# Performance work log

Hardware: AMD Instinct MI355X
Metric: run time of the kernel (lower is better)

Reference implementation:

```python
import jax, jax.numpy as jnp
import numpy as np

DIM = 512
NUM_HEADS = 8
HEAD_DIM = DIM // NUM_HEADS
MAX_SIZE = 128


def setup_inputs() -> dict:
    key = jax.random.key(0)
    ks = jax.random.split(key, 13)
    B, C, H, W = 4, DIM, 128, 128
    inp = {
        "x": jax.random.normal(ks[0], (B, C, H, W), jnp.float32),
        "q_w": jax.random.normal(ks[1], (DIM, DIM), jnp.float32) * 0.02,
        "q_b": jax.random.normal(ks[2], (DIM,), jnp.float32) * 0.02,
        "k_w": jax.random.normal(ks[3], (DIM, DIM), jnp.float32) * 0.02,
        "k_b": jax.random.normal(ks[4], (DIM,), jnp.float32) * 0.02,
        "v_w": jax.random.normal(ks[5], (DIM, DIM), jnp.float32) * 0.02,
        "v_b": jax.random.normal(ks[6], (DIM,), jnp.float32) * 0.02,
        "o_w": jax.random.normal(ks[7], (DIM, DIM), jnp.float32) * 0.02,
        "o_b": jax.random.normal(ks[8], (DIM,), jnp.float32) * 0.02,
        "pos_q": jax.random.normal(ks[9], (1, NUM_HEADS, MAX_SIZE, HEAD_DIM), jnp.float32),
        "pos_k": jax.random.normal(ks[10], (1, NUM_HEADS, MAX_SIZE, HEAD_DIM), jnp.float32),
        "pos_v": jax.random.normal(ks[11], (1, NUM_HEADS, MAX_SIZE, HEAD_DIM), jnp.float32),
        "g_q": jnp.ones((1,), jnp.float32),
        "g_k": jnp.ones((1,), jnp.float32),
        "g_v1": jnp.ones((1,), jnp.float32),
        "g_v2": jnp.ones((1,), jnp.float32),
    }
    return inp


def _gated_axial_attn(x, q_w, q_b, k_w, k_b, v_w, v_b, o_w, o_b,
                      pos_q, pos_k, pos_v, g_q, g_k, g_v1, g_v2):
    B, C, H, W = x.shape
    nh, hd = NUM_HEADS, C // NUM_HEADS
    scale = hd ** (-0.5)
    # axis='width': attend along W for each (B,H) row
    xf = jnp.transpose(x, (0, 2, 3, 1)).reshape(B * H, W, C)  # (BH, W, C)

    def proj(w, b):
        y = xf @ w.T + b                       # (BH, W, C)
        return jnp.transpose(y.reshape(B * H, W, nh, hd), (0, 2, 1, 3))  # (BH, nh, W, hd)

    q = proj(q_w, q_b)
    k = proj(k_w, k_b)
    v = proj(v_w, v_b)

    pq = pos_q[0, :, :W, :]  # (nh, W, hd)
    pk = pos_k[0, :, :W, :]
    pv = pos_v[0, :, :W, :]

    # scores[i,j] = q_i.k_j + g_q * q_i.pq_j + g_k * pk_i.k_j, all scaled
    scores = jnp.einsum('bnid,bnjd->bnij', q, k)
    scores = scores + g_q[0] * jnp.einsum('bnid,njd->bnij', q, pq)
    scores = scores + g_k[0] * jnp.einsum('nid,bnjd->bnij', pk, k)
    attn = jax.nn.softmax(scores * scale, axis=-1)  # (BH, nh, W, W)

    vmix = g_v1[0] * v + g_v2[0] * pv[None]        # (BH, nh, W, hd)
    out = jnp.einsum('bnij,bnjd->bnid', attn, vmix)
    out = jnp.transpose(out, (0, 2, 1, 3)).reshape(B * H, W, C)
    out = out @ o_w.T + o_b
    return jnp.transpose(out.reshape(B, H, W, C), (0, 3, 1, 2))  # (B, C, H, W)


def reference(x, q_w, q_b, k_w, k_b, v_w, v_b, o_w, o_b,
              pos_q, pos_k, pos_v, g_q, g_k, g_v1, g_v2):
    return _gated_axial_attn(x, q_w, q_b, k_w, k_b, v_w, v_b, o_w, o_b,
                             pos_q, pos_k, pos_v, g_q, g_k, g_v1, g_v2)
```

## Files before the change

kernel.cpp:

```cpp
#include <hip/hip_runtime.h>

typedef __bf16 bf16;
typedef __attribute__((ext_vector_type(8))) __bf16 bf16x8;
typedef __attribute__((ext_vector_type(4))) __bf16 bf16x4;
typedef __attribute__((ext_vector_type(4))) float fvec4;

#define MFMA16(a, b, c) __builtin_amdgcn_mfma_f32_16x16x32_bf16(a, b, c, 0, 0, 0)

__device__ __forceinline__ void glds16(const bf16* g, bf16* l) {
  __builtin_amdgcn_global_load_lds(
      (const __attribute__((address_space(1))) void*)g,
      (__attribute__((address_space(3))) void*)l, 16, 0, 0);
}

__device__ inline fvec4 zero4() { fvec4 z = {0.f, 0.f, 0.f, 0.f}; return z; }

#define PREP_ELEMS 1245184

__global__ __launch_bounds__(512) void prep_kernel(
    const float* __restrict__ qw, const float* __restrict__ kw,
    const float* __restrict__ vw, const float* __restrict__ ow,
    const float* __restrict__ pq, const float* __restrict__ pk,
    const float* __restrict__ pv,
    const float* __restrict__ g_q, const float* __restrict__ g_k,
    const float* __restrict__ g_v2, bf16* __restrict__ dst)
{
  int i = (blockIdx.x * 512 + threadIdx.x) * 4;
  const float* s;
  float sc = 1.f;
  if      (i < 262144)  s = qw + i;
  else if (i < 524288)  s = kw + (i - 262144);
  else if (i < 786432)  s = vw + (i - 524288);
  else if (i < 1048576) s = ow + (i - 786432);
  else if (i < 1114112) { s = pq + (i - 1048576); sc = g_q[0]; }
  else if (i < 1179648) { s = pk + (i - 1114112); sc = g_k[0]; }
  else                  { s = pv + (i - 1179648); sc = g_v2[0]; }
  fvec4 v = *(const fvec4*)s;
  bf16x4 o = { (bf16)(v[0] * sc), (bf16)(v[1] * sc),
               (bf16)(v[2] * sc), (bf16)(v[3] * sc) };
  *(bf16x4*)(dst + i) = o;
}

__global__ __launch_bounds__(256) void xpose_kernel(
    const float* __restrict__ x, bf16* __restrict__ xt, int bh0)
{
  __shared__ float Xs[64 * 133];
  const int cb = blockIdx.x, lb = blockIdx.y;
  const int bh = bh0 + lb, b = bh >> 7, h = bh & 127;
  const int t = threadIdx.x;
  const float* xb = x + (size_t)b * 8388608 + (size_t)(cb * 64) * 16384 + h * 128;
  #pragma unroll
  for (int it = 0; it < 8; ++it) {
    int idx = it * 256 + t;
    int c = idx >> 5, w4 = (idx & 31) << 2;
    fvec4 v = *(const fvec4*)(xb + (size_t)c * 16384 + w4);
    #pragma unroll
    for (int j = 0; j < 4; ++j) Xs[c * 133 + w4 + j] = v[j];
  }
  __syncthreads();
  const int c0 = (t & 7) * 8, wsub = t >> 3;
  #pragma unroll
  for (int wb = 0; wb < 4; ++wb) {
    int w = wb * 32 + wsub;
    bf16x8 o;
    #pragma unroll
    for (int i = 0; i < 8; ++i) o[i] = (bf16)Xs[(c0 + i) * 133 + w];
    *(bf16x8*)(xt + ((size_t)lb * 128 + w) * 512 + cb * 64 + c0) = o;
  }
}

__global__ __launch_bounds__(512, 4) void qkvattn_kernel(
    const bf16* __restrict__ xt, const bf16* __restrict__ wqkv,
    const float* __restrict__ q_b, const float* __restrict__ k_b,
    const float* __restrict__ v_b, const bf16* __restrict__ posb,
    const float* __restrict__ g_v1, bf16* __restrict__ ao)
{
  __shared__ bf16 SM[24576];
  bf16* Qs = SM;
  bf16* KP = SM + 8192;
  bf16* Vt = SM;

  const int nwg = gridDim.x;
  int wg = blockIdx.x;
  wg = (wg & 7) * (nwg >> 3) + (wg >> 3);
  const int lb = wg >> 3, n = wg & 7;

  const int t = threadIdx.x;
  const int wv = t >> 6, lane = t & 63;
  const int lr = lane & 15, lg = lane >> 4;
  const int srow = lane >> 3, c16 = lane & 7;
  const int wm2 = wv >> 1, wn2 = wv & 1;

  fvec4 acc[2][6];
  #pragma unroll
  for (int i = 0; i < 2; ++i)
    #pragma unroll
    for (int j = 0; j < 6; ++j) acc[i][j] = zero4();

  const bf16* asrc[2];
  const bf16* bsrc[3];
  #pragma unroll
  for (int j = 0; j < 2; ++j) {
    int seg = wv * 2 + j;
    int row = seg * 8 + srow;
    int cs = c16 ^ (row & 7);
    asrc[j] = xt + (size_t)(lb * 128 + row) * 512 + cs * 8;
  }
  #pragma unroll
  for (int j = 0; j < 3; ++j) {
    int seg = wv * 3 + j;
    int row = seg * 8 + srow;
    int grow = ((row >> 6) << 9) + (n << 6) + (row & 63);
    int cs = c16 ^ (row & 7);
    bsrc[j] = wqkv + (size_t)grow * 512 + cs * 8;
  }

  for (int k0 = 0; k0 < 512; k0 += 64) {
    __syncthreads();
    #pragma unroll
    for (int j = 0; j < 2; ++j) glds16(asrc[j] + k0, SM + (wv * 2 + j) * 512);
    #pragma unroll
    for (int j = 0; j < 3; ++j) glds16(bsrc[j] + k0, SM + 8192 + (wv * 3 + j) * 512);
    __syncthreads();
    #pragma unroll
    for (int kc = 0; kc < 2; ++kc) {
      bf16x8 af[2], bfv[6];
      #pragma unroll
      for (int mt = 0; mt < 2; ++mt) {
        int row = wm2 * 32 + mt * 16 + lr;
        int cs = (kc * 4 + lg) ^ (row & 7);
        af[mt] = *(const bf16x8*)(SM + row * 64 + cs * 8);
      }
      #pragma unroll
      for (int nt = 0; nt < 6; ++nt) {
        int row = wn2 * 96 + nt * 16 + lr;
        int cs = (kc * 4 + lg) ^ (row & 7);
        bfv[nt] = *(const bf16x8*)(SM + 8192 + row * 64 + cs * 8);
      }
      #pragma unroll
      for (int mt = 0; mt < 2; ++mt)
        #pragma unroll
        for (int nt = 0; nt < 6; ++nt)
          acc[mt][nt] = MFMA16(af[mt], bfv[nt], acc[mt][nt]);
    }
  }
  __syncthreads();

  const float gv1 = g_v1[0];
  const bf16* pqb = posb + (size_t)n * 8192;
  const bf16* pkb = posb + 65536 + (size_t)n * 8192;
  const bf16* pvb = posb + 131072 + (size_t)n * 8192;

  #pragma unroll
  for (int mt = 0; mt < 2; ++mt) {
    #pragma unroll
    for (int nt = 0; nt < 6; ++nt) {
      int gc = wn2 * 96 + nt * 16 + lr;
      int sec = gc >> 6;
      int d = gc & 63;
      int rb = wm2 * 32 + mt * 16 + lg * 4;
      if (sec == 0) {
        float bq = q_b[n * 64 + d];
        #pragma unroll
        for (int r = 0; r < 4; ++r) {
          int row = rb + r;
          Qs[row * 64 + (((d >> 3) ^ (row & 7)) << 3) + (d & 7)] =
              (bf16)(acc[mt][nt][r] + bq);
        }
      } else if (sec == 1) {
        float bk = k_b[n * 64 + d];
        #pragma unroll
        for (int r = 0; r < 4; ++r) {
          int row = rb + r;
          float kv = acc[mt][nt][r] + bk;
          KP[row * 128 + (((d >> 3) ^ (row & 7)) << 3) + (d & 7)] =
              (bf16)(kv + (float)pqb[row * 64 + d]);
          int d2 = 64 + d;
          KP[row * 128 + (((d2 >> 3) ^ (row & 7)) << 3) + (d2 & 7)] = (bf16)kv;
        }
      }
    }
  }
  __syncthreads();

  const int i0 = wv * 16;
  fvec4 s[8];
  #pragma unroll
  for (int i = 0; i < 8; ++i) s[i] = zero4();
  #pragma unroll
  for (int kc = 0; kc < 4; ++kc) {
    bf16x8 af;
    if (kc < 2) {
      int row = i0 + lr;
      int cs = (kc * 4 + lg) ^ (row & 7);
      af = *(const bf16x8*)(Qs + row * 64 + cs * 8);
    } else {
      af = *(const bf16x8*)(pkb + (i0 + lr) * 64 + (kc - 2) * 32 + lg * 8);
    }
    #pragma unroll
    for (int jt = 0; jt < 8; ++jt) {
      int row = jt * 16 + lr;
      int cs = (kc * 4 + lg) ^ (row & 7);
      bf16x8 bfr = *(const bf16x8*)(KP + row * 128 + cs * 8);
      s[jt] = MFMA16(af, bfr, s[jt]);
    }
  }

  const float scale = 0.125f;
  float inv[4];
  #pragma unroll
  for (int r = 0; r < 4; ++r) {
    float m = -1e30f;
    #pragma unroll
    for (int jt = 0; jt < 8; ++jt) m = fmaxf(m, s[jt][r]);
    #pragma unroll
    for (int off = 1; off < 16; off <<= 1) m = fmaxf(m, __shfl_xor(m, off));
    float sm = 0.f;
    #pragma unroll
    for (int jt = 0; jt < 8; ++jt) {
      float e = __expf((s[jt][r] - m) * scale);
      s[jt][r] = e;
      sm += e;
    }
    #pragma unroll
    for (int off = 1; off < 16; off <<= 1) sm += __shfl_xor(sm, off);
    inv[r] = 1.f / sm;
  }
  __syncthreads();

  #pragma unroll
  for (int r = 0; r < 4; ++r) {
    int i = i0 + lg * 4 + r;
    #pragma unroll
    for (int jt = 0; jt < 8; ++jt) {
      int j = jt * 16 + lr;
      KP[i * 128 + (((j >> 3) ^ (i & 7)) << 3) + (j & 7)] =
          (bf16)(s[jt][r] * inv[r]);
    }
  }
  if (wn2 == 1) {
    #pragma unroll
    for (int mt = 0; mt < 2; ++mt) {
      #pragma unroll
      for (int nt = 2; nt < 6; ++nt) {
        int d = nt * 16 - 32 + lr;
        float bv = v_b[n * 64 + d];
        #pragma unroll
        for (int r = 0; r < 4; ++r) {
          int j = wm2 * 32 + mt * 16 + lg * 4 + r;
          float vv = gv1 * (acc[mt][nt][r] + bv) + (float)pvb[j * 64 + d];
          Vt[d * 128 + (((j >> 3) ^ (d & 7)) << 3) + (j & 7)] = (bf16)vv;
        }
      }
    }
  }
  __syncthreads();

  fvec4 o[4];
  #pragma unroll
  for (int i = 0; i < 4; ++i) o[i] = zero4();
  #pragma unroll
  for (int kc = 0; kc < 4; ++kc) {
    int prow = i0 + lr;
    int pcs = (kc * 4 + lg) ^ (prow & 7);
    bf16x8 af = *(const bf16x8*)(KP + prow * 128 + pcs * 8);
    #pragma unroll
    for (int dt = 0; dt < 4; ++dt) {
      int vr = dt * 16 + lr;
      int vcs = (kc * 4 + lg) ^ (vr & 7);
      bf16x8 bfr = *(const bf16x8*)(Vt + vr * 128 + vcs * 8);
      o[dt] = MFMA16(af, bfr, o[dt]);
    }
  }
  #pragma unroll
  for (int dt = 0; dt < 4; ++dt) {
    #pragma unroll
    for (int r = 0; r < 4; ++r) {
      int i = i0 + lg * 4 + r;
      ao[((size_t)lb * 128 + i) * 512 + n * 64 + dt * 16 + lr] = (bf16)o[dt][r];
    }
  }
}

__global__ __launch_bounds__(256, 3) void oproj_kernel(
    const bf16* __restrict__ ao, const bf16* __restrict__ wo,
    const float* __restrict__ o_b, float* __restrict__ out, int bh0)
{
  __shared__ bf16 As[128 * 64];
  __shared__ bf16 Bs[128 * 64];
  const int nwg = gridDim.x;
  int wg = blockIdx.x;
  if ((nwg & 7) == 0) wg = (wg & 7) * (nwg >> 3) + (wg >> 3);
  const int ct4 = wg & 3;
  const int lb = wg >> 2;
  const int bh = bh0 + lb, b = bh >> 7, h = bh & 127;
  const int t = threadIdx.x;
  const int wv = t >> 6, lane = t & 63;
  const int lr = lane & 15, lg = lane >> 4;
  const int wm = wv >> 1, wn = wv & 1;
  const int srow = lane >> 3, c16 = lane & 7;

  fvec4 acc[4][4];
  #pragma unroll
  for (int i = 0; i < 4; ++i)
    #pragma unroll
    for (int j = 0; j < 4; ++j) acc[i][j] = zero4();

  for (int k0 = 0; k0 < 512; k0 += 64) {
    __syncthreads();
    #pragma unroll
    for (int j = 0; j < 4; ++j) {
      int seg = wv * 4 + j;
      int row = seg * 8 + srow;
      int cs = c16 ^ (row & 7);
      glds16(wo + (size_t)(ct4 * 128 + row) * 512 + k0 + cs * 8, As + seg * 512);
      glds16(ao + ((size_t)lb * 128 + row) * 512 + k0 + cs * 8, Bs + seg * 512);
    }
    __syncthreads();
    #pragma unroll
    for (int kc = 0; kc < 2; ++kc) {
      bf16x8 af[4], bfv[4];
      #pragma unroll
      for (int mt = 0; mt < 4; ++mt) {
        int row = wm * 64 + mt * 16 + lr;
        int cs = (kc * 4 + lg) ^ (row & 7);
        af[mt] = *(const bf16x8*)(As + row * 64 + cs * 8);
      }
      #pragma unroll
      for (int nt = 0; nt < 4; ++nt) {
        int row = wn * 64 + nt * 16 + lr;
        int cs = (kc * 4 + lg) ^ (row & 7);
        bfv[nt] = *(const bf16x8*)(Bs + row * 64 + cs * 8);
      }
      #pragma unroll
      for (int mt = 0; mt < 4; ++mt)
        #pragma unroll
        for (int nt = 0; nt < 4; ++nt)
          acc[mt][nt] = MFMA16(af[mt], bfv[nt], acc[mt][nt]);
    }
  }
  #pragma unroll
  for (int mt = 0; mt < 4; ++mt) {
    #pragma unroll
    for (int r = 0; r < 4; ++r) {
      int co = ct4 * 128 + wm * 64 + mt * 16 + lg * 4 + r;
      float bv = o_b[co];
      size_t ob = ((size_t)(b * 512 + co) * 128 + h) * 128;
      #pragma unroll
      for (int nt = 0; nt < 4; ++nt) {
        int w = wn * 64 + nt * 16 + lr;
        out[ob + w] = acc[mt][nt][r] + bv;
      }
    }
  }
}

extern "C" void kernel_launch(void* const* d_in, const int* in_sizes, int n_in,
                              void* d_out, int out_size, void* d_ws, size_t ws_size,
                              hipStream_t stream) {
  const float* x    = (const float*)d_in[0];
  const float* q_w  = (const float*)d_in[1];
  const float* q_b  = (const float*)d_in[2];
  const float* k_w  = (const float*)d_in[3];
  const float* k_b  = (const float*)d_in[4];
  const float* v_w  = (const float*)d_in[5];
  const float* v_b  = (const float*)d_in[6];
  const float* o_w  = (const float*)d_in[7];
  const float* o_b  = (const float*)d_in[8];
  const float* pos_q = (const float*)d_in[9];
  const float* pos_k = (const float*)d_in[10];
  const float* pos_v = (const float*)d_in[11];
  const float* g_q  = (const float*)d_in[12];
  const float* g_k  = (const float*)d_in[13];
  const float* g_v1 = (const float*)d_in[14];
  const float* g_v2 = (const float*)d_in[15];
  float* out = (float*)d_out;

  bf16* prep = (bf16*)d_ws;
  bf16* wqkv = prep;
  bf16* wo   = prep + 786432;
  bf16* posb = prep + 1048576;

  bf16* rest = prep + PREP_ELEMS;
  size_t avail = (ws_size > (size_t)PREP_ELEMS * 2) ? ws_size - (size_t)PREP_ELEMS * 2 : 0;
  const size_t per_bh = (size_t)(65536 + 65536) * sizeof(bf16);
  int nbh = (int)(avail / per_bh);
  if (nbh > 512) nbh = 512;
  if (nbh < 1) nbh = 1;

  bf16* xt = rest;
  bf16* ao = xt + (size_t)nbh * 65536;

  prep_kernel<<<608, 512, 0, stream>>>(q_w, k_w, v_w, o_w, pos_q, pos_k, pos_v,
                                       g_q, g_k, g_v2, prep);

  for (int bh0 = 0; bh0 < 512; bh0 += nbh) {
    int cur = (512 - bh0 < nbh) ? (512 - bh0) : nbh;
    xpose_kernel<<<dim3(8, cur), 256, 0, stream>>>(x, xt, bh0);
    qkvattn_kernel<<<cur * 8, 512, 0, stream>>>(xt, wqkv, q_b, k_b, v_b, posb,
                                                g_v1, ao);
    oproj_kernel<<<cur * 4, 256, 0, stream>>>(ao, wo, o_b, out, bh0);
  }
}
```

Measured before the change: 504.2 us.

## Fuse NCHW transpose into QKV GEMM with double-buffered A/B loads

Removes the separate xpose kernel and its bf16 intermediate buffer. The QKV/attention kernel now reads the fp32 NCHW input directly, converts it to bf16 in registers and writes it swizzled into LDS. It also double-buffers the A and B tiles so the next k-chunk loads while the current one feeds MFMA. Each x row is now re-read by all 8 head workgroups instead of once, and LDS use per block grows, which may lower occupancy.

```diff
diff --git a/kernel.cpp b/kernel.cpp
--- a/kernel.cpp
+++ b/kernel.cpp
@@ -41,41 +41,13 @@
   *(bf16x4*)(dst + i) = o;
 }
 
-__global__ __launch_bounds__(256) void xpose_kernel(
-    const float* __restrict__ x, bf16* __restrict__ xt, int bh0)
-{
-  __shared__ float Xs[64 * 133];
-  const int cb = blockIdx.x, lb = blockIdx.y;
-  const int bh = bh0 + lb, b = bh >> 7, h = bh & 127;
-  const int t = threadIdx.x;
-  const float* xb = x + (size_t)b * 8388608 + (size_t)(cb * 64) * 16384 + h * 128;
-  #pragma unroll
-  for (int it = 0; it < 8; ++it) {
-    int idx = it * 256 + t;
-    int c = idx >> 5, w4 = (idx & 31) << 2;
-    fvec4 v = *(const fvec4*)(xb + (size_t)c * 16384 + w4);
-    #pragma unroll
-    for (int j = 0; j < 4; ++j) Xs[c * 133 + w4 + j] = v[j];
-  }
-  __syncthreads();
-  const int c0 = (t & 7) * 8, wsub = t >> 3;
-  #pragma unroll
-  for (int wb = 0; wb < 4; ++wb) {
-    int w = wb * 32 + wsub;
-    bf16x8 o;
-    #pragma unroll
-    for (int i = 0; i < 8; ++i) o[i] = (bf16)Xs[(c0 + i) * 133 + w];
-    *(bf16x8*)(xt + ((size_t)lb * 128 + w) * 512 + cb * 64 + c0) = o;
-  }
-}
-
 __global__ __launch_bounds__(512, 4) void qkvattn_kernel(
-    const bf16* __restrict__ xt, const bf16* __restrict__ wqkv,
+    const float* __restrict__ x, const bf16* __restrict__ wqkv,
     const float* __restrict__ q_b, const float* __restrict__ k_b,
     const float* __restrict__ v_b, const bf16* __restrict__ posb,
-    const float* __restrict__ g_v1, bf16* __restrict__ ao)
+    const float* __restrict__ g_v1, bf16* __restrict__ ao, int bh0)
 {
-  __shared__ bf16 SM[24576];
+  __shared__ bf16 SM[40960];
   bf16* Qs = SM;
   bf16* KP = SM + 8192;
   bf16* Vt = SM;
@@ -84,6 +56,7 @@
   int wg = blockIdx.x;
   wg = (wg & 7) * (nwg >> 3) + (wg >> 3);
   const int lb = wg >> 3, n = wg & 7;
+  const int bh = bh0 + lb, bb = bh >> 7, hh = bh & 127;
 
   const int t = threadIdx.x;
   const int wv = t >> 6, lane = t & 63;
@@ -97,15 +70,11 @@
     #pragma unroll
     for (int j = 0; j < 6; ++j) acc[i][j] = zero4();
 
-  const bf16* asrc[2];
+  const int wl = t & 63, ac0 = (t >> 6) << 3;
+  const float* xA = x + (size_t)bb * 8388608 + (size_t)ac0 * 16384 + hh * 128;
+  float ar[16];
+
   const bf16* bsrc[3];
-  #pragma unroll
-  for (int j = 0; j < 2; ++j) {
-    int seg = wv * 2 + j;
-    int row = seg * 8 + srow;
-    int cs = c16 ^ (row & 7);
-    asrc[j] = xt + (size_t)(lb * 128 + row) * 512 + cs * 8;
-  }
   #pragma unroll
   for (int j = 0; j < 3; ++j) {
     int seg = wv * 3 + j;
@@ -115,13 +84,45 @@
     bsrc[j] = wqkv + (size_t)grow * 512 + cs * 8;
   }
 
+#define LOADA(k0)                                                   \
+  {                                                                 \
+    const float* p = xA + (size_t)(k0) * 16384;                     \
+    _Pragma("unroll")                                               \
+    for (int i = 0; i < 8; ++i) {                                   \
+      ar[i]     = p[(size_t)i * 16384 + wl];                        \
+      ar[8 + i] = p[(size_t)i * 16384 + wl + 64];                   \
+    }                                                               \
+  }
+#define WRITEA(Ad)                                                  \
+  {                                                                 \
+    _Pragma("unroll")                                               \
+    for (int g = 0; g < 2; ++g) {                                   \
+      int w = wl + g * 64;                                          \
+      bf16x8 v;                                                     \
+      _Pragma("unroll")                                             \
+      for (int i = 0; i < 8; ++i) v[i] = (bf16)ar[g * 8 + i];       \
+      int oc = (ac0 >> 3) ^ (w & 7);                                \
+      *(bf16x8*)((Ad) + w * 64 + oc * 8) = v;                       \
+    }                                                               \
+  }
+
+  LOADA(0);
+  #pragma unroll
+  for (int j = 0; j < 3; ++j) glds16(bsrc[j], SM + 8192 + (wv * 3 + j) * 512);
+  WRITEA(SM);
+  __syncthreads();
+
+  int cur = 0;
   for (int k0 = 0; k0 < 512; k0 += 64) {
-    __syncthreads();
-    #pragma unroll
-    for (int j = 0; j < 2; ++j) glds16(asrc[j] + k0, SM + (wv * 2 + j) * 512);
-    #pragma unroll
-    for (int j = 0; j < 3; ++j) glds16(bsrc[j] + k0, SM + 8192 + (wv * 3 + j) * 512);
-    __syncthreads();
+    bf16* nb = SM + (cur ^ 1) * 20480;
+    if (k0 < 448) {
+      LOADA(k0 + 64);
+      #pragma unroll
+      for (int j = 0; j < 3; ++j)
+        glds16(bsrc[j] + k0 + 64, nb + 8192 + (wv * 3 + j) * 512);
+    }
+    const bf16* Ab = SM + cur * 20480;
+    const bf16* Bb = Ab + 8192;
     #pragma unroll
     for (int kc = 0; kc < 2; ++kc) {
       bf16x8 af[2], bfv[6];
@@ -129,13 +130,13 @@
       for (int mt = 0; mt < 2; ++mt) {
         int row = wm2 * 32 + mt * 16 + lr;
         int cs = (kc * 4 + lg) ^ (row & 7);
-        af[mt] = *(const bf16x8*)(SM + row * 64 + cs * 8);
+        af[mt] = *(const bf16x8*)(Ab + row * 64 + cs * 8);
       }
       #pragma unroll
       for (int nt = 0; nt < 6; ++nt) {
         int row = wn2 * 96 + nt * 16 + lr;
         int cs = (kc * 4 + lg) ^ (row & 7);
-        bfv[nt] = *(const bf16x8*)(SM + 8192 + row * 64 + cs * 8);
+        bfv[nt] = *(const bf16x8*)(Bb + row * 64 + cs * 8);
       }
       #pragma unroll
       for (int mt = 0; mt < 2; ++mt)
@@ -143,8 +144,12 @@
         for (int nt = 0; nt < 6; ++nt)
           acc[mt][nt] = MFMA16(af[mt], bfv[nt], acc[mt][nt]);
     }
-  }
-  __syncthreads();
+    if (k0 < 448) WRITEA(nb);
+    __syncthreads();
+    cur ^= 1;
+  }
+#undef LOADA
+#undef WRITEA
 
   const float gv1 = g_v1[0];
   const bf16* pqb = posb + (size_t)n * 8192;
@@ -383,22 +388,20 @@
 
   bf16* rest = prep + PREP_ELEMS;
   size_t avail = (ws_size > (size_t)PREP_ELEMS * 2) ? ws_size - (size_t)PREP_ELEMS * 2 : 0;
-  const size_t per_bh = (size_t)(65536 + 65536) * sizeof(bf16);
+  const size_t per_bh = (size_t)65536 * sizeof(bf16);
   int nbh = (int)(avail / per_bh);
   if (nbh > 512) nbh = 512;
   if (nbh < 1) nbh = 1;
 
-  bf16* xt = rest;
-  bf16* ao = xt + (size_t)nbh * 65536;
+  bf16* ao = rest;
 
   prep_kernel<<<608, 512, 0, stream>>>(q_w, k_w, v_w, o_w, pos_q, pos_k, pos_v,
                                        g_q, g_k, g_v2, prep);
 
   for (int bh0 = 0; bh0 < 512; bh0 += nbh) {
     int cur = (512 - bh0 < nbh) ? (512 - bh0) : nbh;
-    xpose_kernel<<<dim3(8, cur), 256, 0, stream>>>(x, xt, bh0);
-    qkvattn_kernel<<<cur * 8, 512, 0, stream>>>(xt, wqkv, q_b, k_b, v_b, posb,
-                                                g_v1, ao);
+    qkvattn_kernel<<<cur * 8, 512, 0, stream>>>(x, wqkv, q_b, k_b, v_b, posb,
+                                                g_v1, ao, bh0);
     oproj_kernel<<<cur * 4, 256, 0, stream>>>(ao, wo, o_b, out, bh0);
   }
 }
```

Result: faster. 482.9 us (-4.2%).
